# Performance work log

Measured on AMD Instinct MI355X. Metric: run time of the kernel, lower is better.

Reference implementation:

```python
import jax, jax.numpy as jnp
import numpy as np

B, F, D, C, K = 131072, 32, 16, 64, 8  # batch, features, qsvt degree, classes, KAN grid
CLIP = 1.0 - 1e-6


def setup_inputs() -> dict:
    key = jax.random.key(0)
    ks = jax.random.split(key, 7)
    return {
        "X": jax.random.normal(ks[0], (B, F), jnp.float32),
        "qsvt_phases": 0.1 * jax.random.normal(ks[1], (D,), jnp.float32),
        "lcu_weights": jax.random.uniform(ks[2], (F, D), jnp.float32),
        "sum_scale": jnp.ones((F,), jnp.float32) + 0.1 * jax.random.normal(ks[3], (F,), jnp.float32),
        "sum_bias": 0.1 * jax.random.normal(ks[4], (F,), jnp.float32),
        "kan_coeff": jax.random.normal(ks[5], (C, F, K), jnp.float32) / np.sqrt(F * K),
        "kan_bias": jnp.zeros((C,), jnp.float32),
    }


def reference(X, qsvt_phases, lcu_weights, sum_scale, sum_bias, kan_coeff, kan_bias):
    # QSVT: Chebyshev-with-phases polynomial features of each scalar input,
    # vectorized over (batch, feature) instead of the original Python loops.
    degree = qsvt_phases.shape[0]
    grid = kan_coeff.shape[-1]
    theta = jnp.arccos(jnp.clip(X, -CLIP, CLIP))                  # [B,F]
    kd = jnp.arange(1, degree + 1, dtype=X.dtype)                 # [D]
    qsvt_vecs = jnp.cos(theta[..., None] * kd + qsvt_phases)      # [B,F,D]
    # LCU block: normalized linear combination over the degree axis -> scalar per (b,f)
    lcu = jnp.sum(qsvt_vecs * lcu_weights, axis=-1) / (
        jnp.sum(jnp.abs(lcu_weights), axis=-1) + 1e-6)            # [B,F]
    # QuantumSumBlock (one per feature): per-feature affine + tanh squash
    feat = jnp.tanh(sum_scale * lcu + sum_bias)                   # [B,F]
    # KAN layer: Chebyshev basis expansion then per-(class,feature,basis) coefficients
    t2 = jnp.arccos(jnp.clip(feat, -CLIP, CLIP))                  # [B,F]
    kk = jnp.arange(grid, dtype=X.dtype)                          # [K]
    basis = jnp.cos(t2[..., None] * kk)                           # [B,F,K]
    return jnp.einsum('bfk,cfk->bc', basis, kan_coeff) + kan_bias  # [B,C]
```

## Files before the change

kernel.cpp:

```cpp
#include <hip/hip_runtime.h>

#define F 32
#define Dd 16
#define C 64
#define Kk 8
#define CLIPV (1.0f - 1e-6f)
#define CHUNKU 536
#define K2 2.8853900817779268f
#define NBLK 1024
#define MT 2

typedef short v8s __attribute__((ext_vector_type(8)));
typedef float v4f __attribute__((ext_vector_type(4)));
typedef float v2f __attribute__((ext_vector_type(2)));

static __device__ inline unsigned cvtpk(float lo, float hi) {
    unsigned r;
    asm("v_cvt_pk_bf16_f32 %0, %1, %2" : "=v"(r) : "v"(lo), "v"(hi));
    return r;
}

#define BAR_WRITES() do {                                        \
    asm volatile("s_waitcnt lgkmcnt(0)" ::: "memory");           \
    __builtin_amdgcn_s_barrier();                                \
    asm volatile("" ::: "memory");                               \
} while (0)
#define BAR_READS() do {                                         \
    asm volatile("" ::: "memory");                               \
    __builtin_amdgcn_s_barrier();                                \
    asm volatile("" ::: "memory");                               \
} while (0)

__global__ __launch_bounds__(256, 4) void qkan_kernel(
    const float* __restrict__ X,
    const float* __restrict__ phases,
    const float* __restrict__ lcu_w,
    const float* __restrict__ sscale,
    const float* __restrict__ sbias,
    const float* __restrict__ coeff,
    const float* __restrict__ kbias,
    float* __restrict__ out)
{
    __shared__ unsigned short s_basis[F * CHUNKU];

    const int tid = threadIdx.x;
    const int lane = tid & 63;
    const int wu = __builtin_amdgcn_readfirstlane(tid >> 6);
    const int h = lane >> 4;
    const int r16 = lane & 15;
    const int fe = tid & 31;
    const int rg = tid >> 5;

    const int rb0 = blockIdx.x * (MT * 64);

    float xq[8];
    {
        const float* xp = X + (size_t)(rb0 + rg * 8) * F + fe;
#pragma unroll
        for (int m = 0; m < 8; ++m) xq[m] = xp[m * F];
    }

    v2f cc[16];
    float fbias;
    {
        const float* lwf = lcu_w + fe * Dd;
        float wv[16];
        float asum = 0.f;
#pragma unroll
        for (int d = 0; d < Dd; ++d) {
            wv[d] = lwf[d];
            asum += fabsf(wv[d]);
        }
        const float sc = K2 * sscale[fe] / (asum + 1e-6f);
#pragma unroll
        for (int d = 0; d < Dd; ++d) {
            float sp, cp;
            __sincosf(phases[d], &sp, &cp);
            cc[d][0] = sc * wv[d] * cp;
            cc[d][1] = -sc * wv[d] * sp;
        }
        fbias = K2 * sbias[fe];
    }

    v8s Bfr[8];
    const int cidx = wu * 16 + r16;
#pragma unroll
    for (int q = 0; q < 8; ++q) {
        const float* gp = coeff + ((size_t)(cidx * F + 4 * q + h) * Kk);
        const float4 g0 = *reinterpret_cast<const float4*>(gp);
        const float4 g1 = *reinterpret_cast<const float4*>(gp + 4);
        union { unsigned u[4]; v8s v; } bb;
        bb.u[0] = cvtpk(g0.x, g0.y);
        bb.u[1] = cvtpk(g0.z, g0.w);
        bb.u[2] = cvtpk(g1.x, g1.y);
        bb.u[3] = cvtpk(g1.z, g1.w);
        Bfr[q] = bb.v;
    }
    const float biasreg = kbias[cidx];

    for (int mt = 0; mt < MT; ++mt) {
        const int row_base = rb0 + mt * 64;
        if (mt) BAR_READS();

        float xn[8];
        if (mt + 1 < MT) {
            const float* xp = X + (size_t)(row_base + 64 + rg * 8) * F + fe;
#pragma unroll
            for (int m = 0; m < 8; ++m) xn[m] = xp[m * F];
        }

#pragma unroll
        for (int m = 0; m < 8; ++m) {
            const int row = rg * 8 + m;
            const float x = fminf(fmaxf(xq[m], -CLIPV), CLIPV);
            const float s1 = sqrtf(fmaxf(__builtin_fmaf(-x, x, 1.f), 0.f));
            const float tx = x + x;
            const v2f tx2 = {tx, tx};
            v2f w = {0.f, 0.f}, wp = {0.f, 0.f};
#pragma unroll
            for (int j = 15; j >= 0; --j) {
                const v2f wn = (cc[j] - wp) + tx2 * w;
                wp = w;
                w = wn;
            }
            float z = fbias - wp[0];
            z = __builtin_fmaf(x, w[0], z);
            z = __builtin_fmaf(s1, w[1], z);
            float e;
            asm("v_exp_f32 %0, %1" : "=v"(e) : "v"(z));
            const float rr = __builtin_amdgcn_rcpf(e + 1.f);
            const float t = __builtin_fmaf(-2.f, rr, 1.f);
            const float t2 = t + t;
            const float b1 = t;
            const float b2 = t2 * b1 - 1.f;
            const float b3 = t2 * b2 - b1;
            const float b4 = t2 * b3 - b2;
            const float b5 = t2 * b4 - b3;
            const float b6 = t2 * b5 - b4;
            const float b7 = t2 * b6 - b5;
            uint4 pk;
            pk.x = cvtpk(1.f, b1);
            pk.y = cvtpk(b2, b3);
            pk.z = cvtpk(b4, b5);
            pk.w = cvtpk(b6, b7);
            *reinterpret_cast<uint4*>(&s_basis[fe * CHUNKU + row * 8]) = pk;
        }
        BAR_WRITES();

#pragma unroll
        for (int t = 0; t < 4; ++t) {
            v4f acc = {0.f, 0.f, 0.f, 0.f};
#pragma unroll
            for (int q = 0; q < 8; ++q) {
                const v8s a = *reinterpret_cast<const v8s*>(
                    &s_basis[(4 * q + h) * CHUNKU + (t * 16 + r16) * 8]);
                acc = __builtin_amdgcn_mfma_f32_16x16x32_bf16(a, Bfr[q], acc, 0, 0, 0);
            }
            const int row0 = row_base + t * 16 + h * 4;
#pragma unroll
            for (int i = 0; i < 4; ++i) {
                out[(size_t)(row0 + i) * C + cidx] = acc[i] + biasreg;
            }
        }

        if (mt + 1 < MT) {
#pragma unroll
            for (int m = 0; m < 8; ++m) xq[m] = xn[m];
        }
    }
}

extern "C" void kernel_launch(void* const* d_in, const int* in_sizes, int n_in,
                              void* d_out, int out_size, void* d_ws, size_t ws_size,
                              hipStream_t stream) {
    const float* X  = (const float*)d_in[0];
    const float* ph = (const float*)d_in[1];
    const float* lw = (const float*)d_in[2];
    const float* ss = (const float*)d_in[3];
    const float* sb = (const float*)d_in[4];
    const float* kc = (const float*)d_in[5];
    const float* kb = (const float*)d_in[6];
    float* out = (float*)d_out;
    qkan_kernel<<<dim3(NBLK), dim3(256), 0, stream>>>(X, ph, lw, ss, sb, kc, kb, out);
}
```

Before: 27.17 us.

## Process one 64-row tile per block and XOR-swizzle LDS basis layout

Each block now handles a single 64-row tile, doubling the grid to 2048 blocks and removing the two-tile loop with its X prefetch and second barrier. The padded LDS stride is replaced by a 512-element stride with an XOR swizzle on row and feature indices, meant to avoid bank conflicts on both the writes and the MFMA operand reads without padding. In exchange, each block's per-block setup (coefficient fragments, LCU constants) is amortised over half as many rows.

```diff
diff --git a/kernel.cpp b/kernel.cpp
--- a/kernel.cpp
+++ b/kernel.cpp
@@ -5,10 +5,8 @@
 #define C 64
 #define Kk 8
 #define CLIPV (1.0f - 1e-6f)
-#define CHUNKU 536
 #define K2 2.8853900817779268f
-#define NBLK 1024
-#define MT 2
+#define NBLK 2048
 
 typedef short v8s __attribute__((ext_vector_type(8)));
 typedef float v4f __attribute__((ext_vector_type(4)));
@@ -25,11 +23,6 @@
     __builtin_amdgcn_s_barrier();                                \
     asm volatile("" ::: "memory");                               \
 } while (0)
-#define BAR_READS() do {                                         \
-    asm volatile("" ::: "memory");                               \
-    __builtin_amdgcn_s_barrier();                                \
-    asm volatile("" ::: "memory");                               \
-} while (0)
 
 __global__ __launch_bounds__(256, 4) void qkan_kernel(
     const float* __restrict__ X,
@@ -41,7 +34,7 @@
     const float* __restrict__ kbias,
     float* __restrict__ out)
 {
-    __shared__ unsigned short s_basis[F * CHUNKU];
+    __shared__ unsigned short s_basis[F * 512];
 
     const int tid = threadIdx.x;
     const int lane = tid & 63;
@@ -49,13 +42,14 @@
     const int h = lane >> 4;
     const int r16 = lane & 15;
     const int fe = tid & 31;
+    const int fe7 = fe & 7;
     const int rg = tid >> 5;
 
-    const int rb0 = blockIdx.x * (MT * 64);
+    const int rb = blockIdx.x * 64;
 
     float xq[8];
     {
-        const float* xp = X + (size_t)(rb0 + rg * 8) * F + fe;
+        const float* xp = X + (size_t)(rb + rg * 8) * F + fe;
 #pragma unroll
         for (int m = 0; m < 8; ++m) xq[m] = xp[m * F];
     }
@@ -98,74 +92,58 @@
     }
     const float biasreg = kbias[cidx];
 
-    for (int mt = 0; mt < MT; ++mt) {
-        const int row_base = rb0 + mt * 64;
-        if (mt) BAR_READS();
-
-        float xn[8];
-        if (mt + 1 < MT) {
-            const float* xp = X + (size_t)(row_base + 64 + rg * 8) * F + fe;
 #pragma unroll
-            for (int m = 0; m < 8; ++m) xn[m] = xp[m * F];
+    for (int m = 0; m < 8; ++m) {
+        const float x = fminf(fmaxf(xq[m], -CLIPV), CLIPV);
+        const float s1 = sqrtf(fmaxf(__builtin_fmaf(-x, x, 1.f), 0.f));
+        const float tx = x + x;
+        const v2f tx2 = {tx, tx};
+        v2f w = {0.f, 0.f}, wp = {0.f, 0.f};
+#pragma unroll
+        for (int j = 15; j >= 0; --j) {
+            const v2f wn = (cc[j] - wp) + tx2 * w;
+            wp = w;
+            w = wn;
         }
+        float z = fbias - wp[0];
+        z = __builtin_fmaf(x, w[0], z);
+        z = __builtin_fmaf(s1, w[1], z);
+        float e;
+        asm("v_exp_f32 %0, %1" : "=v"(e) : "v"(z));
+        const float rr = __builtin_amdgcn_rcpf(e + 1.f);
+        const float t = __builtin_fmaf(-2.f, rr, 1.f);
+        const float t2 = t + t;
+        const float b1 = t;
+        const float b2 = t2 * b1 - 1.f;
+        const float b3 = t2 * b2 - b1;
+        const float b4 = t2 * b3 - b2;
+        const float b5 = t2 * b4 - b3;
+        const float b6 = t2 * b5 - b4;
+        const float b7 = t2 * b6 - b5;
+        uint4 pk;
+        pk.x = cvtpk(1.f, b1);
+        pk.y = cvtpk(b2, b3);
+        pk.z = cvtpk(b4, b5);
+        pk.w = cvtpk(b6, b7);
+        *reinterpret_cast<uint4*>(
+            &s_basis[fe * 512 + rg * 64 + ((m ^ fe7) << 3)]) = pk;
+    }
+    BAR_WRITES();
 
 #pragma unroll
-        for (int m = 0; m < 8; ++m) {
-            const int row = rg * 8 + m;
-            const float x = fminf(fmaxf(xq[m], -CLIPV), CLIPV);
-            const float s1 = sqrtf(fmaxf(__builtin_fmaf(-x, x, 1.f), 0.f));
-            const float tx = x + x;
-            const v2f tx2 = {tx, tx};
-            v2f w = {0.f, 0.f}, wp = {0.f, 0.f};
+    for (int t = 0; t < 4; ++t) {
+        const int s0 = ((t * 16 + r16) ^ h) << 3;
+        v4f acc = {0.f, 0.f, 0.f, 0.f};
 #pragma unroll
-            for (int j = 15; j >= 0; --j) {
-                const v2f wn = (cc[j] - wp) + tx2 * w;
-                wp = w;
-                w = wn;
-            }
-            float z = fbias - wp[0];
-            z = __builtin_fmaf(x, w[0], z);
-            z = __builtin_fmaf(s1, w[1], z);
-            float e;
-            asm("v_exp_f32 %0, %1" : "=v"(e) : "v"(z));
-            const float rr = __builtin_amdgcn_rcpf(e + 1.f);
-            const float t = __builtin_fmaf(-2.f, rr, 1.f);
-            const float t2 = t + t;
-            const float b1 = t;
-            const float b2 = t2 * b1 - 1.f;
-            const float b3 = t2 * b2 - b1;
-            const float b4 = t2 * b3 - b2;
-            const float b5 = t2 * b4 - b3;
-            const float b6 = t2 * b5 - b4;
-            const float b7 = t2 * b6 - b5;
-            uint4 pk;
-            pk.x = cvtpk(1.f, b1);
-            pk.y = cvtpk(b2, b3);
-            pk.z = cvtpk(b4, b5);
-            pk.w = cvtpk(b6, b7);
-            *reinterpret_cast<uint4*>(&s_basis[fe * CHUNKU + row * 8]) = pk;
+        for (int q = 0; q < 8; ++q) {
+            const int idx = (4 * q + h) * 512 + (s0 ^ ((q & 1) << 5));
+            const v8s a = *reinterpret_cast<const v8s*>(&s_basis[idx]);
+            acc = __builtin_amdgcn_mfma_f32_16x16x32_bf16(a, Bfr[q], acc, 0, 0, 0);
         }
-        BAR_WRITES();
-
+        const int row0 = rb + t * 16 + h * 4;
 #pragma unroll
-        for (int t = 0; t < 4; ++t) {
-            v4f acc = {0.f, 0.f, 0.f, 0.f};
-#pragma unroll
-            for (int q = 0; q < 8; ++q) {
-                const v8s a = *reinterpret_cast<const v8s*>(
-                    &s_basis[(4 * q + h) * CHUNKU + (t * 16 + r16) * 8]);
-                acc = __builtin_amdgcn_mfma_f32_16x16x32_bf16(a, Bfr[q], acc, 0, 0, 0);
-            }
-            const int row0 = row_base + t * 16 + h * 4;
-#pragma unroll
-            for (int i = 0; i < 4; ++i) {
-                out[(size_t)(row0 + i) * C + cidx] = acc[i] + biasreg;
-            }
-        }
-
-        if (mt + 1 < MT) {
-#pragma unroll
-            for (int m = 0; m < 8; ++m) xq[m] = xn[m];
+        for (int i = 0; i < 4; ++i) {
+            out[(size_t)(row0 + i) * C + cidx] = acc[i] + biasreg;
         }
     }
 }
```

After: 27.84 us. 1.02x slower.
